# Kernel tuning notes

Measured on AMD Instinct MI355X. Metric: run time of the kernel, lower is better.

The kernel has to match this reference:

```python
import jax, jax.numpy as jnp
import numpy as np

N = 100000   # nodes
E = 1600000  # edges (avg degree 16)
D = 64       # channels (in = hidden = out)
L = 3        # layers


def setup_inputs() -> dict:
    key = jax.random.key(0)
    ks = jax.random.split(key, 8)
    s = 1.0 / np.sqrt(D)
    x = jax.random.normal(ks[0], (N, D), jnp.float32)
    edge_index = jax.random.randint(ks[1], (2, E), 0, N, dtype=jnp.int32)
    edge_type = jax.random.randint(ks[2], (E,), 0, 5, dtype=jnp.int32)
    Wq = jax.random.normal(ks[3], (L, D, D), jnp.float32) * s
    Wk = jax.random.normal(ks[4], (L, D, D), jnp.float32) * s
    Wv = jax.random.normal(ks[5], (L, D, D), jnp.float32) * s
    Ws = jax.random.normal(ks[6], (L, D, D), jnp.float32) * s
    bq = jnp.zeros((L, D), jnp.float32)
    bk = jnp.zeros((L, D), jnp.float32)
    bv = jnp.zeros((L, D), jnp.float32)
    bs = jnp.zeros((L, D), jnp.float32)
    return {"x": x, "edge_index": edge_index, "edge_type": edge_type,
            "Wq": Wq, "bq": bq, "Wk": Wk, "bk": bk,
            "Wv": Wv, "bv": bv, "Ws": Ws, "bs": bs}


def _transformer_conv(x, src, dst, Wq, bq, Wk, bk, Wv, bv, Ws, bs):
    # PyG TransformerConv, heads=1, concat=True, root_weight=True, beta=False
    q = x @ Wq + bq            # [N, D]
    k = x @ Wk + bk            # [N, D]
    v = x @ Wv + bv            # [N, D]
    scale = 1.0 / jnp.sqrt(jnp.asarray(D, x.dtype))
    # per-edge attention logits: <q_i, k_j> / sqrt(D)
    alpha = jnp.sum(q[dst] * k[src], axis=-1) * scale   # [E]
    # scatter-softmax over incoming edges of each target node
    m = jax.ops.segment_max(alpha, dst, num_segments=N)  # [N]
    e = jnp.exp(alpha - m[dst])                          # [E]
    denom = jax.ops.segment_sum(e, dst, num_segments=N)  # [N]
    a = e / (denom[dst] + 1e-16)                         # [E]
    # scatter-add aggregation of alpha * v_j
    agg = jax.ops.segment_sum(a[:, None] * v[src], dst, num_segments=N)  # [N, D]
    # root/skip connection (lin_skip with bias)
    return agg + x @ Ws + bs


def reference(x, edge_index, edge_type, Wq, bq, Wk, bk, Wv, bv, Ws, bs):
    src, dst = edge_index[0], edge_index[1]
    h = x
    for i in range(L):
        h = _transformer_conv(h, src, dst, Wq[i], bq[i], Wk[i], bk[i],
                              Wv[i], bv[i], Ws[i], bs[i])
        if i < L - 1:
            h = jax.nn.relu(h)
            # F.dropout(p=0.4) is identity in eval mode
    return h
```

## Files before the change

### kernel.cpp

```cpp
#include <hip/hip_runtime.h>

#define D 64
#define LAYERS 3
#define BSHIFT 8
#define NBMAX 512
#define CHUNK 4096
#define WSTRIDE 72

typedef unsigned short ushort_t;
typedef __bf16 bf16x8 __attribute__((ext_vector_type(8)));
typedef float f32x4 __attribute__((ext_vector_type(4)));

__device__ __forceinline__ ushort_t f2bf(float f) {
    unsigned b = __float_as_uint(f);
    b += 0x7FFFu + ((b >> 16) & 1u);
    return (ushort_t)(b >> 16);
}
__device__ __forceinline__ float bflo(unsigned u) { return __uint_as_float(u << 16); }
__device__ __forceinline__ float bfhi(unsigned u) { return __uint_as_float(u & 0xFFFF0000u); }

__global__ __launch_bounds__(256) void proj_kernel(
    const float* __restrict__ x,
    const float* __restrict__ Wq, const float* __restrict__ bq,
    const float* __restrict__ Wk, const float* __restrict__ bk,
    const float* __restrict__ Wv, const float* __restrict__ bv,
    const float* __restrict__ Ws, const float* __restrict__ bs,
    float* __restrict__ q, ushort_t* __restrict__ kv,
    float* __restrict__ hout, int N)
{
    __shared__ ushort_t xs[32 * WSTRIDE];
    __shared__ ushort_t wt[4 * 64 * WSTRIDE];

    const int t = threadIdx.x;
    const int block_row = blockIdx.x * 32;

    {
        const int r  = t >> 3;
        const int c8 = (t & 7) * 8;
        const int row = block_row + r;
        float4 x0, x1;
        if (row < N) {
            x0 = *(const float4*)(x + (size_t)row * D + c8);
            x1 = *(const float4*)(x + (size_t)row * D + c8 + 4);
        } else {
            x0 = make_float4(0.f,0.f,0.f,0.f); x1 = x0;
        }
        uint4 u;
        u.x = (unsigned)f2bf(x0.x) | ((unsigned)f2bf(x0.y) << 16);
        u.y = (unsigned)f2bf(x0.z) | ((unsigned)f2bf(x0.w) << 16);
        u.z = (unsigned)f2bf(x1.x) | ((unsigned)f2bf(x1.y) << 16);
        u.w = (unsigned)f2bf(x1.z) | ((unsigned)f2bf(x1.w) << 16);
        *(uint4*)(xs + r * WSTRIDE + c8) = u;
    }
    {
        const float* Wm[4] = {Wq, Wk, Wv, Ws};
#pragma unroll
        for (int m = 0; m < 4; ++m) {
            const float* W = Wm[m];
            ushort_t* wtm = wt + m * 64 * WSTRIDE;
#pragma unroll
            for (int i = 0; i < 16; ++i) {
                const int e = i * 256 + t;
                const int k = e >> 6, n = e & 63;
                wtm[n * WSTRIDE + k] = f2bf(W[e]);
            }
        }
    }
    __syncthreads();

    const int l  = t & 63;
    const int w  = t >> 6;
    const int lr = l & 15;
    const int lk = (l >> 4) * 8;

    bf16x8 afr[2][2];
#pragma unroll
    for (int rt = 0; rt < 2; ++rt)
#pragma unroll
        for (int ks = 0; ks < 2; ++ks)
            afr[rt][ks] = *(const bf16x8*)(xs + (rt*16 + lr) * WSTRIDE + ks*32 + lk);

    const ushort_t* wtw = wt + w * 64 * WSTRIDE;
    f32x4 acc[2][4];
#pragma unroll
    for (int rt = 0; rt < 2; ++rt)
#pragma unroll
        for (int ct = 0; ct < 4; ++ct)
            acc[rt][ct] = (f32x4){0.f, 0.f, 0.f, 0.f};

#pragma unroll
    for (int ct = 0; ct < 4; ++ct) {
        const bf16x8 b0 = *(const bf16x8*)(wtw + (ct*16 + lr) * WSTRIDE + lk);
        const bf16x8 b1 = *(const bf16x8*)(wtw + (ct*16 + lr) * WSTRIDE + 32 + lk);
        acc[0][ct] = __builtin_amdgcn_mfma_f32_16x16x32_bf16(afr[0][0], b0, acc[0][ct], 0, 0, 0);
        acc[0][ct] = __builtin_amdgcn_mfma_f32_16x16x32_bf16(afr[0][1], b1, acc[0][ct], 0, 0, 0);
        acc[1][ct] = __builtin_amdgcn_mfma_f32_16x16x32_bf16(afr[1][0], b0, acc[1][ct], 0, 0, 0);
        acc[1][ct] = __builtin_amdgcn_mfma_f32_16x16x32_bf16(afr[1][1], b1, acc[1][ct], 0, 0, 0);
    }

    const float* biasW = (w == 0) ? bq : (w == 1) ? bk : (w == 2) ? bv : bs;
    float bcol[4];
#pragma unroll
    for (int ct = 0; ct < 4; ++ct) bcol[ct] = biasW[ct*16 + lr];

#pragma unroll
    for (int rt = 0; rt < 2; ++rt) {
#pragma unroll
        for (int ct = 0; ct < 4; ++ct) {
#pragma unroll
            for (int r = 0; r < 4; ++r) {
                const int row = block_row + rt*16 + (l >> 4) * 4 + r;
                const int col = ct*16 + lr;
                if (row < N) {
                    const float val = acc[rt][ct][r] + bcol[ct];
                    if (w == 0)      q[(size_t)row * D + col]    = val;
                    else if (w == 3) hout[(size_t)row * D + col] = val;
                    else {
                        ushort_t* kvr = kv + (size_t)row * 128;
                        kvr[(col >> 2) * 8 + ((w == 2) ? 4 : 0) + (col & 3)] = f2bf(val);
                    }
                }
            }
        }
    }
}

__global__ __launch_bounds__(256) void b_hist_kernel(
    const int* __restrict__ dst, int* __restrict__ bcount, int E)
{
    __shared__ int h[NBMAX];
    const int t = threadIdx.x;
    h[t] = 0; h[t + 256] = 0;
    __syncthreads();
    const int base = blockIdx.x * CHUNK;
#pragma unroll
    for (int i = 0; i < 16; ++i) {
        const int e = base + i * 256 + t;
        if (e < E) atomicAdd(h + (dst[e] >> BSHIFT), 1);
    }
    __syncthreads();
    if (h[t])       atomicAdd(bcount + t, h[t]);
    if (h[t + 256]) atomicAdd(bcount + t + 256, h[t + 256]);
}

__global__ __launch_bounds__(512) void b_scan_kernel(
    const int* __restrict__ bcount, int* __restrict__ bbase,
    int* __restrict__ gcursor, int E)
{
    __shared__ int tmp[NBMAX];
    const int t = threadIdx.x;
    const int val = bcount[t];
    tmp[t] = val;
    __syncthreads();
    for (int off = 1; off < NBMAX; off <<= 1) {
        int x = (t >= off) ? tmp[t - off] : 0;
        __syncthreads();
        tmp[t] += x;
        __syncthreads();
    }
    const int excl = tmp[t] - val;
    bbase[t] = excl;
    gcursor[t] = excl;
    if (t == NBMAX - 1) bbase[NBMAX] = E;
}

__global__ __launch_bounds__(256) void b_scatter_kernel(
    const int* __restrict__ src, const int* __restrict__ dst,
    int* __restrict__ gcursor, uint2* __restrict__ packed, int E)
{
    __shared__ int h[NBMAX];
    __shared__ int gb[NBMAX];
    const int t = threadIdx.x;
    h[t] = 0; h[t + 256] = 0;
    __syncthreads();

    const int base = blockIdx.x * CHUNK;
    int ls[16], ld[16], lr[16];
#pragma unroll
    for (int i = 0; i < 16; ++i) {
        const int e = base + i * 256 + t;
        if (e < E) {
            ls[i] = src[e];
            ld[i] = dst[e];
            lr[i] = atomicAdd(h + (ld[i] >> BSHIFT), 1);
        }
    }
    __syncthreads();
    for (int b = t; b < NBMAX; b += 256) {
        const int c = h[b];
        gb[b] = c ? atomicAdd(gcursor + b, c) : 0;
    }
    __syncthreads();
#pragma unroll
    for (int i = 0; i < 16; ++i) {
        const int e = base + i * 256 + t;
        if (e < E) {
            const int pos = gb[ld[i] >> BSHIFT] + lr[i];
            packed[pos] = make_uint2((unsigned)ls[i], (unsigned)ld[i]);
        }
    }
}

__global__ __launch_bounds__(256) void b_final_kernel(
    const uint2* __restrict__ packed, const int* __restrict__ bbase,
    int* __restrict__ esrc, int* __restrict__ offs, int* __restrict__ counts,
    int N)
{
    __shared__ int hist[256];
    __shared__ int scan[256];
    __shared__ int cursor[256];
    const int t = threadIdx.x;
    const int b = blockIdx.x;
    const int s = bbase[b];
    const int e = bbase[b + 1];

    hist[t] = 0;
    __syncthreads();
    for (int j = s + t; j < e; j += 256) {
        atomicAdd(hist + (packed[j].y & 255), 1);
    }
    __syncthreads();
    const int val = hist[t];
    scan[t] = val;
    __syncthreads();
    for (int off = 1; off < 256; off <<= 1) {
        int x = (t >= off) ? scan[t - off] : 0;
        __syncthreads();
        scan[t] += x;
        __syncthreads();
    }
    const int excl = scan[t] - val;
    const int node = b * 256 + t;
    if (node < N) {
        counts[node] = val;
        offs[node]   = s + excl;
    }
    cursor[t] = excl;
    __syncthreads();
    for (int j = s + t; j < e; j += 256) {
        const uint2 p = packed[j];
        const int r = atomicAdd(cursor + (p.y & 255), 1);
        esrc[s + r] = (int)p.x;
    }
}

__global__ __launch_bounds__(256) void node_kernel(
    const float* __restrict__ q, const uint4* __restrict__ kv,
    const int* __restrict__ esrc, const int* __restrict__ offs,
    const int* __restrict__ counts, float* __restrict__ hout,
    int N, int do_relu)
{
    const int t = threadIdx.x;
    const int lane = t & 15;
    const int node = blockIdx.x * 16 + (t >> 4);
    if (node >= N) return;

    const int start = offs[node];
    const int end   = start + counts[node];

    const float4 qv = *(const float4*)(q + (size_t)node * D + lane * 4);

    float m = -INFINITY, ssum = 0.0f;
    float4 acc = make_float4(0.0f, 0.0f, 0.0f, 0.0f);

    int j = start;
    for (; j + 2 <= end; j += 2) {
        const int s0 = esrc[j];
        const int s1 = esrc[j + 1];
        const uint4 u0 = kv[(size_t)s0 * 16 + lane];
        const uint4 u1 = kv[(size_t)s1 * 16 + lane];

        float p0 = bflo(u0.x) * qv.x + bfhi(u0.x) * qv.y
                 + bflo(u0.y) * qv.z + bfhi(u0.y) * qv.w;
        float p1 = bflo(u1.x) * qv.x + bfhi(u1.x) * qv.y
                 + bflo(u1.y) * qv.z + bfhi(u1.y) * qv.w;
        p0 += __shfl_xor(p0, 1);  p1 += __shfl_xor(p1, 1);
        p0 += __shfl_xor(p0, 2);  p1 += __shfl_xor(p1, 2);
        p0 += __shfl_xor(p0, 4);  p1 += __shfl_xor(p1, 4);
        p0 += __shfl_xor(p0, 8);  p1 += __shfl_xor(p1, 8);
        p0 *= 0.125f;  p1 *= 0.125f;

        const float mx = fmaxf(p0, p1);
        if (mx > m) {
            const float sc = __expf(m - mx);
            ssum *= sc;
            acc.x *= sc; acc.y *= sc; acc.z *= sc; acc.w *= sc;
            m = mx;
        }
        const float w0 = __expf(p0 - m);
        const float w1 = __expf(p1 - m);
        ssum += w0 + w1;
        acc.x = fmaf(w0, bflo(u0.z), fmaf(w1, bflo(u1.z), acc.x));
        acc.y = fmaf(w0, bfhi(u0.z), fmaf(w1, bfhi(u1.z), acc.y));
        acc.z = fmaf(w0, bflo(u0.w), fmaf(w1, bflo(u1.w), acc.z));
        acc.w = fmaf(w0, bfhi(u0.w), fmaf(w1, bfhi(u1.w), acc.w));
    }
    if (j < end) {
        const int s0 = esrc[j];
        const uint4 u0 = kv[(size_t)s0 * 16 + lane];
        float p0 = bflo(u0.x) * qv.x + bfhi(u0.x) * qv.y
                 + bflo(u0.y) * qv.z + bfhi(u0.y) * qv.w;
        p0 += __shfl_xor(p0, 1);
        p0 += __shfl_xor(p0, 2);
        p0 += __shfl_xor(p0, 4);
        p0 += __shfl_xor(p0, 8);
        p0 *= 0.125f;
        if (p0 > m) {
            const float sc = __expf(m - p0);
            ssum *= sc;
            acc.x *= sc; acc.y *= sc; acc.z *= sc; acc.w *= sc;
            m = p0;
        }
        const float w0 = __expf(p0 - m);
        ssum += w0;
        acc.x = fmaf(w0, bflo(u0.z), acc.x);
        acc.y = fmaf(w0, bfhi(u0.z), acc.y);
        acc.z = fmaf(w0, bflo(u0.w), acc.z);
        acc.w = fmaf(w0, bfhi(u0.w), acc.w);
    }

    const float inv = 1.0f / (ssum + 1e-16f);
    float* o = hout + (size_t)node * D + lane * 4;
    float4 ov = *(const float4*)o;
    ov.x = fmaf(acc.x, inv, ov.x);
    ov.y = fmaf(acc.y, inv, ov.y);
    ov.z = fmaf(acc.z, inv, ov.z);
    ov.w = fmaf(acc.w, inv, ov.w);
    if (do_relu) {
        ov.x = fmaxf(ov.x, 0.0f); ov.y = fmaxf(ov.y, 0.0f);
        ov.z = fmaxf(ov.z, 0.0f); ov.w = fmaxf(ov.w, 0.0f);
    }
    *(float4*)o = ov;
}

extern "C" void kernel_launch(void* const* d_in, const int* in_sizes, int n_in,
                              void* d_out, int out_size, void* d_ws, size_t ws_size,
                              hipStream_t stream)
{
    const float* x   = (const float*)d_in[0];
    const int* ei    = (const int*)d_in[1];
    const float* Wq  = (const float*)d_in[3];
    const float* bq  = (const float*)d_in[4];
    const float* Wk  = (const float*)d_in[5];
    const float* bk  = (const float*)d_in[6];
    const float* Wv  = (const float*)d_in[7];
    const float* bv  = (const float*)d_in[8];
    const float* Ws  = (const float*)d_in[9];
    const float* bs  = (const float*)d_in[10];

    const int N = in_sizes[0] / D;
    const int E = in_sizes[2];
    const int* src = ei;
    const int* dst = ei + E;
    const int NB = (N + 255) / 256;

    float* fws = (float*)d_ws;
    float* q     = fws;
    ushort_t* kv = (ushort_t*)(q + (size_t)N * D);
    float* h0    = (float*)(kv + (size_t)N * 128);
    float* h1    = h0 + (size_t)N * D;
    int* esrc    = (int*)(h1 + (size_t)N * D);
    uint2* packed = (uint2*)(esrc + E);
    int* counts  = (int*)(packed + E);
    int* offs    = counts + NBMAX * 256;
    int* bcount  = offs + NBMAX * 256;
    int* bbase   = bcount + NBMAX;
    int* gcursor = bbase + NBMAX + 1;

    hipMemsetAsync(bcount, 0, NBMAX * 4, stream);
    const int p1_blocks = (E + CHUNK - 1) / CHUNK;
    b_hist_kernel<<<p1_blocks, 256, 0, stream>>>(dst, bcount, E);
    b_scan_kernel<<<1, NBMAX, 0, stream>>>(bcount, bbase, gcursor, E);
    b_scatter_kernel<<<p1_blocks, 256, 0, stream>>>(src, dst, gcursor, packed, E);
    b_final_kernel<<<NB, 256, 0, stream>>>(packed, bbase, esrc, offs, counts, N);

    const int proj_blocks = (N + 31) / 32;
    const int node_blocks = (N + 15) / 16;

    const float* cur = x;
    for (int l = 0; l < LAYERS; ++l) {
        float* hout = (l == LAYERS - 1) ? (float*)d_out : (l & 1 ? h1 : h0);

        proj_kernel<<<proj_blocks, 256, 0, stream>>>(
            cur,
            Wq + (size_t)l * D * D, bq + (size_t)l * D,
            Wk + (size_t)l * D * D, bk + (size_t)l * D,
            Wv + (size_t)l * D * D, bv + (size_t)l * D,
            Ws + (size_t)l * D * D, bs + (size_t)l * D,
            q, kv, hout, N);

        node_kernel<<<node_blocks, 256, 0, stream>>>(
            q, (const uint4*)kv, esrc, offs, counts, hout, N,
            l < LAYERS - 1 ? 1 : 0);

        cur = hout;
    }
}
```

Before: 363.1 us.

## Sort nodes by in-degree to balance per-wave work in node kernel

```diff
diff --git a/kernel.cpp b/kernel.cpp
--- a/kernel.cpp
+++ b/kernel.cpp
@@ -6,6 +6,7 @@
 #define NBMAX 512
 #define CHUNK 4096
 #define WSTRIDE 72
+#define DBINS 128
 
 typedef unsigned short ushort_t;
 typedef __bf16 bf16x8 __attribute__((ext_vector_type(8)));
@@ -244,16 +245,58 @@
     }
 }
 
+__global__ __launch_bounds__(256) void deg_hist_kernel(
+    const int* __restrict__ counts, int* __restrict__ dh, int N)
+{
+    __shared__ int h[DBINS];
+    const int t = threadIdx.x;
+    if (t < DBINS) h[t] = 0;
+    __syncthreads();
+    const int i = blockIdx.x * 256 + t;
+    if (i < N) atomicAdd(h + min(counts[i], DBINS - 1), 1);
+    __syncthreads();
+    if (t < DBINS && h[t]) atomicAdd(dh + t, h[t]);
+}
+
+__global__ __launch_bounds__(DBINS) void deg_scan_kernel(
+    const int* __restrict__ dh, int* __restrict__ dcur)
+{
+    __shared__ int tmp[DBINS];
+    const int t = threadIdx.x;
+    const int val = dh[t];
+    tmp[t] = val;
+    __syncthreads();
+    for (int off = 1; off < DBINS; off <<= 1) {
+        int x = (t >= off) ? tmp[t - off] : 0;
+        __syncthreads();
+        tmp[t] += x;
+        __syncthreads();
+    }
+    dcur[t] = tmp[t] - val;
+}
+
+__global__ __launch_bounds__(256) void deg_scatter_kernel(
+    const int* __restrict__ counts, int* __restrict__ dcur,
+    int* __restrict__ perm, int N)
+{
+    const int i = blockIdx.x * 256 + threadIdx.x;
+    if (i >= N) return;
+    const int d = min(counts[i], DBINS - 1);
+    const int pos = atomicAdd(dcur + d, 1);
+    perm[pos] = i;
+}
+
 __global__ __launch_bounds__(256) void node_kernel(
     const float* __restrict__ q, const uint4* __restrict__ kv,
     const int* __restrict__ esrc, const int* __restrict__ offs,
-    const int* __restrict__ counts, float* __restrict__ hout,
-    int N, int do_relu)
+    const int* __restrict__ counts, const int* __restrict__ perm,
+    float* __restrict__ hout, int N, int do_relu)
 {
     const int t = threadIdx.x;
     const int lane = t & 15;
-    const int node = blockIdx.x * 16 + (t >> 4);
-    if (node >= N) return;
+    const int idx = blockIdx.x * 16 + (t >> 4);
+    if (idx >= N) return;
+    const int node = perm[idx];
 
     const int start = offs[node];
     const int end   = start + counts[node];
@@ -366,13 +409,20 @@
     int* bcount  = offs + NBMAX * 256;
     int* bbase   = bcount + NBMAX;
     int* gcursor = bbase + NBMAX + 1;
+    int* perm    = gcursor + NBMAX;
+    int* dh      = perm + N;
+    int* dcur    = dh + DBINS;
 
     hipMemsetAsync(bcount, 0, NBMAX * 4, stream);
+    hipMemsetAsync(dh, 0, DBINS * 4, stream);
     const int p1_blocks = (E + CHUNK - 1) / CHUNK;
     b_hist_kernel<<<p1_blocks, 256, 0, stream>>>(dst, bcount, E);
     b_scan_kernel<<<1, NBMAX, 0, stream>>>(bcount, bbase, gcursor, E);
     b_scatter_kernel<<<p1_blocks, 256, 0, stream>>>(src, dst, gcursor, packed, E);
     b_final_kernel<<<NB, 256, 0, stream>>>(packed, bbase, esrc, offs, counts, N);
+    deg_hist_kernel<<<(N + 255) / 256, 256, 0, stream>>>(counts, dh, N);
+    deg_scan_kernel<<<1, DBINS, 0, stream>>>(dh, dcur);
+    deg_scatter_kernel<<<(N + 255) / 256, 256, 0, stream>>>(counts, dcur, perm, N);
 
     const int proj_blocks = (N + 31) / 32;
     const int node_blocks = (N + 15) / 16;
@@ -390,7 +440,7 @@
             q, kv, hout, N);
 
         node_kernel<<<node_blocks, 256, 0, stream>>>(
-            q, (const uint4*)kv, esrc, offs, counts, hout, N,
+            q, (const uint4*)kv, esrc, offs, counts, perm, hout, N,
             l < LAYERS - 1 ? 1 : 0);
 
         cur = hout;
```

Result: slower. 661.6 us (+82.2%).
